# Performance work log

Measured on AMD Instinct MI355X. Metric: run time of the kernel, lower is better.

Reference implementation:

```python
import jax, jax.numpy as jnp
import numpy as np

ALPHA = 0.2  # leaky relu slope
NEG = -1e9


def setup_inputs() -> dict:
    key = jax.random.key(0)
    ks = jax.random.split(key, 8)
    B, N, F_IN, H, HID, OUT = 2, 4096, 512, 4, 128, 64
    x = jax.random.normal(ks[0], (B, N, F_IN), dtype=jnp.float32)
    adj = jax.random.randint(ks[1], (B, N, N), 0, 2, dtype=jnp.int32)
    s_in = float(np.sqrt(2.0 / (F_IN + HID)))
    W_heads = jax.random.normal(ks[2], (H, HID, F_IN), dtype=jnp.float32) * s_in
    a1_heads = jax.random.normal(ks[3], (H, HID), dtype=jnp.float32) * 0.1
    a2_heads = jax.random.normal(ks[4], (H, HID), dtype=jnp.float32) * 0.1
    s_out = float(np.sqrt(2.0 / (H * HID + OUT)))
    W_out = jax.random.normal(ks[5], (OUT, H * HID), dtype=jnp.float32) * s_out
    a1_out = jax.random.normal(ks[6], (OUT,), dtype=jnp.float32) * 0.1
    a2_out = jax.random.normal(ks[7], (OUT,), dtype=jnp.float32) * 0.1
    return {"x": x, "adj": adj, "W_heads": W_heads, "a1_heads": a1_heads,
            "a2_heads": a2_heads, "W_out": W_out, "a1_out": a1_out, "a2_out": a2_out}


def _gat_layer(x, adj, W, a1, a2, concat):
    # x: [B,N,F], W: [O,F], a1/a2: [O]
    h = jnp.einsum('bnf,of->bno', x, W)            # [B,N,O]
    f1 = jnp.einsum('bno,o->bn', h, a1)            # [B,N]
    f2 = jnp.einsum('bno,o->bn', h, a2)            # [B,N]
    e = f1[:, :, None] + f2[:, None, :]            # [B,N,N] additive scores
    e = jnp.where(e > 0, e, ALPHA * e)             # leaky relu
    e = jnp.where(adj == 0, NEG, e)                # adjacency mask
    att = jax.nn.softmax(e, axis=2)
    h_prime = jnp.einsum('bnm,bmo->bno', att, h)
    return jax.nn.elu(h_prime) if concat else h_prime


def reference(x, adj, W_heads, a1_heads, a2_heads, W_out, a1_out, a2_out):
    H = W_heads.shape[0]
    heads = [_gat_layer(x, adj, W_heads[i], a1_heads[i], a2_heads[i], True)
             for i in range(H)]
    x_cat = jnp.concatenate(heads, axis=2)         # [B,N,H*HID]
    return _gat_layer(x_cat, adj, W_out, a1_out, a2_out, False)
```

## Files before the change

kernel.cpp:

```cpp
#include <hip/hip_runtime.h>

#define TB 2
#define TN 4096
#define TH 4
#define THID 128
#define TOUT 64
#define NW 128

using f4    = __attribute__((ext_vector_type(4))) float;
using s16x8 = __attribute__((ext_vector_type(8))) short;
using s16x4 = __attribute__((ext_vector_type(4))) short;
using u32x4 = __attribute__((ext_vector_type(4))) unsigned;

static __device__ __forceinline__ short f2bf(float f){
  unsigned u = __float_as_uint(f);
  unsigned r = u + 0x7FFFu + ((u >> 16) & 1u);
  return (short)(r >> 16);
}
static __device__ __forceinline__ float bf2f(short s){
  return __uint_as_float(((unsigned)(unsigned short)s) << 16);
}
static __device__ __forceinline__ unsigned encf(float f){
  unsigned u = __float_as_uint(f);
  return (u & 0x80000000u) ? ~u : (u | 0x80000000u);
}
static __device__ __forceinline__ float decf(unsigned u){
  unsigned v = (u & 0x80000000u) ? (u & 0x7FFFFFFFu) : ~u;
  return __uint_as_float(v);
}
static __device__ __forceinline__ void gll16(const void* g, void* l){
  __builtin_amdgcn_global_load_lds((const __attribute__((address_space(1))) unsigned int*)g,
                                   (__attribute__((address_space(3))) unsigned int*)l, 16, 0, 0);
}
static __device__ __forceinline__ f4 mfma_bf16(s16x8 a, s16x8 b, f4 c){
  return __builtin_amdgcn_mfma_f32_16x16x32_bf16(a, b, c, 0, 0, 0);
}

__global__ void k_pack(const int* __restrict__ adj, unsigned* __restrict__ adjp){
  int t = blockIdx.x * 256 + threadIdx.x;
  const int4* p = (const int4*)adj + (size_t)t * 8;
  unsigned m = 0;
#pragma unroll
  for (int i = 0; i < 8; ++i){
    int4 v = p[i];
    m |= (v.x != 0 ? 1u : 0u) << (i*4+0);
    m |= (v.y != 0 ? 1u : 0u) << (i*4+1);
    m |= (v.z != 0 ? 1u : 0u) << (i*4+2);
    m |= (v.w != 0 ? 1u : 0u) << (i*4+3);
  }
  adjp[t] = m;
}

__global__ void k_split(const float* __restrict__ x, short* __restrict__ hi, short* __restrict__ lo){
  int t = blockIdx.x * 256 + threadIdx.x;
  f4 v = ((const f4*)x)[t];
  s16x4 h, l;
#pragma unroll
  for (int e = 0; e < 4; ++e){
    short hb = f2bf(v[e]);
    h[e] = hb;
    l[e] = f2bf(v[e] - bf2f(hb));
  }
  ((s16x4*)hi)[t] = h;
  ((s16x4*)lo)[t] = l;
}
__global__ void k_cvt(const float* __restrict__ x, short* __restrict__ o){
  int t = blockIdx.x * 256 + threadIdx.x;
  f4 v = ((const f4*)x)[t];
  s16x4 h;
#pragma unroll
  for (int e = 0; e < 4; ++e) h[e] = f2bf(v[e]);
  ((s16x4*)o)[t] = h;
}

__global__ __launch_bounds__(512, 2) void k_gemm1(
    const short* __restrict__ xh, const short* __restrict__ xl,
    const short* __restrict__ wh, const short* __restrict__ wl,
    const float* __restrict__ a1h, const float* __restrict__ a2h,
    short* __restrict__ hTb, float* __restrict__ f1g,
    float* __restrict__ Qa, float* __restrict__ Sa, unsigned* __restrict__ mx){
  __shared__ short tiles[2][4][8192];
  __shared__ float red[2][128][2];
  __shared__ float bmx[2];
  int tid = threadIdx.x, lane = tid & 63, w = tid >> 6;
  int kgrp = lane >> 4, li = lane & 15;
  int nblk = blockIdx.x >> 6, mblk = blockIdx.x & 63;
  int n0 = nblk * 128, m0 = mblk * 128;
  int wn = w >> 2, wm = w & 3;
  const f4 fz = {0.f, 0.f, 0.f, 0.f};
  f4 acc[4][2];
#pragma unroll
  for (int i = 0; i < 4; ++i)
#pragma unroll
    for (int j = 0; j < 2; ++j) acc[i][j] = fz;

#pragma unroll
  for (int tno = 0; tno < 4; ++tno){
    const short* gb = (tno==0 ? wh : tno==1 ? wl : tno==2 ? xh : xl);
    int r0 = (tno < 2) ? n0 : m0;
#pragma unroll
    for (int i = 0; i < 2; ++i){
      int s = (i*8 + w)*64 + lane;
      int row = s >> 3, c = s & 7, cs = c ^ (row & 7);
      gll16(gb + (size_t)(r0 + row)*512 + cs*8, (char*)tiles[0][tno] + (i*8+w)*1024);
    }
  }
  asm volatile("s_waitcnt vmcnt(0)" ::: "memory");
  __syncthreads();

  for (int kt = 0; kt < 8; ++kt){
    int cur = kt & 1;
    if (kt < 7){
      int k0 = (kt+1) * 64;
#pragma unroll
      for (int tno = 0; tno < 4; ++tno){
        const short* gb = (tno==0 ? wh : tno==1 ? wl : tno==2 ? xh : xl);
        int r0 = (tno < 2) ? n0 : m0;
#pragma unroll
        for (int i = 0; i < 2; ++i){
          int s = (i*8 + w)*64 + lane;
          int row = s >> 3, c = s & 7, cs = c ^ (row & 7);
          gll16(gb + (size_t)(r0 + row)*512 + k0 + cs*8, (char*)tiles[cur^1][tno] + (i*8+w)*1024);
        }
      }
    }
    const char* t0 = (const char*)tiles[cur][0];
    const char* t1 = (const char*)tiles[cur][1];
    const char* t2 = (const char*)tiles[cur][2];
    const char* t3 = (const char*)tiles[cur][3];
#pragma unroll
    for (int ks = 0; ks < 2; ++ks){
      int ck = ks*4 + kgrp;
      s16x8 ah[4], al[4], bh[2], bl[2];
#pragma unroll
      for (int fn = 0; fn < 4; ++fn){
        int row = wn*64 + fn*16 + li;
        int off = row*128 + ((ck ^ (row & 7)) << 4);
        ah[fn] = *(const s16x8*)(t0 + off);
        al[fn] = *(const s16x8*)(t1 + off);
      }
#pragma unroll
      for (int fm = 0; fm < 2; ++fm){
        int row = wm*32 + fm*16 + li;
        int off = row*128 + ((ck ^ (row & 7)) << 4);
        bh[fm] = *(const s16x8*)(t2 + off);
        bl[fm] = *(const s16x8*)(t3 + off);
      }
#pragma unroll
      for (int fn = 0; fn < 4; ++fn)
#pragma unroll
        for (int fm = 0; fm < 2; ++fm)
          acc[fn][fm] = mfma_bf16(ah[fn], bh[fm], acc[fn][fm]);
#pragma unroll
      for (int fn = 0; fn < 4; ++fn)
#pragma unroll
        for (int fm = 0; fm < 2; ++fm)
          acc[fn][fm] = mfma_bf16(ah[fn], bl[fm], acc[fn][fm]);
#pragma unroll
      for (int fn = 0; fn < 4; ++fn)
#pragma unroll
        for (int fm = 0; fm < 2; ++fm)
          acc[fn][fm] = mfma_bf16(al[fn], bh[fm], acc[fn][fm]);
    }
    asm volatile("s_waitcnt vmcnt(0)" ::: "memory");
    __syncthreads();
  }
  int head = nblk;
#pragma unroll
  for (int fn = 0; fn < 4; ++fn){
#pragma unroll
    for (int fm = 0; fm < 2; ++fm){
#pragma unroll
      for (int r = 0; r < 4; ++r){
        int nout = n0 + wn*64 + fn*16 + kgrp*4 + r;
        int m = m0 + wm*32 + fm*16 + li;
        int b = m >> 12, n = m & 4095;
        int hid = nout & 127;
        size_t idx = ((size_t)((b*TH + head)*THID + hid))*TN + n;
        hTb[idx] = f2bf(acc[fn][fm][r]);
      }
    }
  }
  const float* a1p = a1h + head*THID;
  const float* a2p = a2h + head*THID;
  float s1[2] = {0.f, 0.f}, s2[2] = {0.f, 0.f};
#pragma unroll
  for (int fn = 0; fn < 4; ++fn)
#pragma unroll
    for (int r = 0; r < 4; ++r){
      int row = wn*64 + fn*16 + kgrp*4 + r;
      float w1 = a1p[row], w2 = a2p[row];
#pragma unroll
      for (int fm = 0; fm < 2; ++fm){
        s1[fm] = fmaf(acc[fn][fm][r], w1, s1[fm]);
        s2[fm] = fmaf(acc[fn][fm][r], w2, s2[fm]);
      }
    }
#pragma unroll
  for (int fm = 0; fm < 2; ++fm){
    s1[fm] += __shfl_xor(s1[fm], 16); s1[fm] += __shfl_xor(s1[fm], 32);
    s2[fm] += __shfl_xor(s2[fm], 16); s2[fm] += __shfl_xor(s2[fm], 32);
  }
  if (kgrp == 0){
#pragma unroll
    for (int fm = 0; fm < 2; ++fm){
      int col = wm*32 + fm*16 + li;
      red[wn][col][0] = s1[fm];
      red[wn][col][1] = s2[fm];
    }
  }
  __syncthreads();
  if (tid < 128){
    float f1v = red[0][tid][0] + red[1][tid][0];
    float f2v = red[0][tid][1] + red[1][tid][1];
    int m = m0 + tid, b = m >> 12, n = m & 4095;
    int idx = (b*TH + head)*TN + n;
    f1g[idx] = f1v;
    Qa[idx] = expf(f2v);
    Sa[idx] = expf(0.2f*f2v);
    float wmx = f2v;
#pragma unroll
    for (int d = 1; d < 64; d <<= 1) wmx = fmaxf(wmx, __shfl_xor(wmx, d));
    if ((tid & 63) == 0) bmx[tid >> 6] = wmx;
  }
  __syncthreads();
  if (tid == 0){
    int b = m0 >> 12;
    atomicMax(&mx[b*TH + head], encf(fmaxf(bmx[0], bmx[1])));
  }
}

__global__ __launch_bounds__(256, 2) void k_attn1(
    const short* __restrict__ hTb, const float* __restrict__ f1,
    const float* __restrict__ Qa, const float* __restrict__ Sa,
    const unsigned* __restrict__ adjp, const unsigned* __restrict__ mx,
    float* __restrict__ part, float* __restrict__ sums){
  __shared__ short tile[2][8192];
  __shared__ float Qs[2048], Ss[2048];
  int tid = threadIdx.x, lane = tid & 63, w = tid >> 6;
  int kgrp = lane >> 4, li = lane & 15;
  int bid = blockIdx.x;
  int js = bid >> 8, b = (bid >> 7) & 1, h = (bid >> 5) & 3, rblk = bid & 31;
  int bh = b*TH + h;
  int jbase = js * 2048;
  const short* hbase = hTb + ((size_t)bh*THID)*TN;

#pragma unroll
  for (int i = 0; i < 2; ++i){
    gll16(Qa + (size_t)bh*TN + jbase + (i*4+w)*256 + lane*4, (char*)Qs + (i*4+w)*1024);
    gll16(Sa + (size_t)bh*TN + jbase + (i*4+w)*256 + lane*4, (char*)Ss + (i*4+w)*1024);
  }
#pragma unroll
  for (int i = 0; i < 4; ++i){
    int s = (i*4 + w)*64 + lane;
    int row = s >> 3, c = s & 7, cs = c ^ (row & 7);
    gll16(hbase + (size_t)row*TN + jbase + cs*8, (char*)tile[0] + (i*4+w)*1024);
  }
  int r0 = rblk*128 + w*32;
  float Pv[2], Rv[2];
  int rowa[2];
  float mf = decf(mx[bh]);
#pragma unroll
  for (int rf = 0; rf < 2; ++rf){
    int row = r0 + rf*16 + li;
    rowa[rf] = row;
    float f1v = f1[bh*TN + row];
    float e = f1v + mf;
    float m = e > 0.f ? e : 0.2f*e;
    Pv[rf] = expf(f1v - m);
    Rv[rf] = expf(0.2f*f1v - m);
  }
  const f4 fz = {0.f,0.f,0.f,0.f};
  f4 acc[2][8];
#pragma unroll
  for (int i = 0; i < 2; ++i)
#pragma unroll
    for (int j = 0; j < 8; ++j) acc[i][j] = fz;
  f4 accs[2] = {fz, fz};
  s16x8 ones;
#pragma unroll
  for (int e = 0; e < 8; ++e) ones[e] = (short)0x3F80;

  uint2 awc[2], awn[2];
#pragma unroll
  for (int rf = 0; rf < 2; ++rf)
    awc[rf] = *(const uint2*)&adjp[(size_t)(b*TN + rowa[rf])*NW + (jbase >> 5)];

  asm volatile("s_waitcnt vmcnt(0)" ::: "memory");
  __syncthreads();

  for (int jt = 0; jt < 32; ++jt){
    int cur = jt & 1;
    if (jt < 31){
      int jg = jbase + (jt+1)*64;
#pragma unroll
      for (int i = 0; i < 4; ++i){
        int s = (i*4 + w)*64 + lane;
        int row = s >> 3, c = s & 7, cs = c ^ (row & 7);
        gll16(hbase + (size_t)row*TN + jg + cs*8, (char*)tile[cur^1] + (i*4+w)*1024);
      }
    }
    int jn = jt < 31 ? jt+1 : jt;
#pragma unroll
    for (int rf = 0; rf < 2; ++rf)
      awn[rf] = *(const uint2*)&adjp[(size_t)(b*TN + rowa[rf])*NW + ((jbase + jn*64) >> 5)];
    int j0 = jt*64;
    const char* tp = (const char*)tile[cur];
#pragma unroll
    for (int ks = 0; ks < 2; ++ks){
      int jloc = j0 + ks*32 + kgrp*8;
      float qv[8], sv[8];
      *(f4*)&qv[0] = *(const f4*)&Qs[jloc];
      *(f4*)&qv[4] = *(const f4*)&Qs[jloc+4];
      *(f4*)&sv[0] = *(const f4*)&Ss[jloc];
      *(f4*)&sv[4] = *(const f4*)&Ss[jloc+4];
      s16x8 af[2];
#pragma unroll
      for (int rf = 0; rf < 2; ++rf){
        unsigned word = ks ? awc[rf].y : awc[rf].x;
        unsigned byt = (word >> (kgrp*8)) & 0xFFu;
        float P = Pv[rf], R = Rv[rf];
        u32x4 pw;
#pragma unroll
        for (int pe = 0; pe < 4; ++pe){
          float va = fmaxf(P*qv[2*pe],   R*sv[2*pe]);
          float vb = fmaxf(P*qv[2*pe+1], R*sv[2*pe+1]);
          va = (byt & (1u << (2*pe)))   ? va : 0.f;
          vb = (byt & (1u << (2*pe+1))) ? vb : 0.f;
          unsigned ua = __float_as_uint(va) + 0x8000u;
          unsigned ub = __float_as_uint(vb) + 0x8000u;
          pw[pe] = __builtin_amdgcn_perm(ub, ua, 0x07060302);
        }
        af[rf] = __builtin_bit_cast(s16x8, pw);
      }
      accs[0] = mfma_bf16(af[0], ones, accs[0]);
      accs[1] = mfma_bf16(af[1], ones, accs[1]);
#pragma unroll
      for (int cf = 0; cf < 8; ++cf){
        int col = cf*16 + li;
        int off = col*128 + (((ks*4 + kgrp) ^ (col & 7)) << 4);
        s16x8 bfr = *(const s16x8*)(tp + off);
        acc[0][cf] = mfma_bf16(af[0], bfr, acc[0][cf]);
        acc[1][cf] = mfma_bf16(af[1], bfr, acc[1][cf]);
      }
    }
    asm volatile("s_waitcnt vmcnt(0)" ::: "memory");
    __syncthreads();
    awc[0] = awn[0]; awc[1] = awn[1];
  }
  int sl = js*8 + bh;
  if (li == 0){
#pragma unroll
    for (int rf = 0; rf < 2; ++rf)
#pragma unroll
      for (int r = 0; r < 4; ++r)
        sums[(size_t)sl*TN + r0 + rf*16 + kgrp*4 + r] = accs[rf][r];
  }
#pragma unroll
  for (int rf = 0; rf < 2; ++rf)
#pragma unroll
    for (int cf = 0; cf < 8; ++cf)
#pragma unroll
      for (int r = 0; r < 4; ++r){
        int row = r0 + rf*16 + kgrp*4 + r;
        int hid = cf*16 + li;
        part[((size_t)sl*TN + row)*THID + hid] = acc[rf][cf][r];
      }
}

__global__ void k_comb1(const float* __restrict__ part, const float* __restrict__ sums,
                        short* __restrict__ xcat){
  int t = blockIdx.x*256 + threadIdx.x;
  int hid4 = t & 31, n = (t >> 5) & 4095, h = (t >> 17) & 3, b = t >> 19;
  int bh = b*TH + h;
  size_t rowoff = (size_t)bh*TN + n;
  size_t rowoff2 = (size_t)(8 + bh)*TN + n;
  f4 p0 = ((const f4*)part)[rowoff*32 + hid4];
  f4 p1 = ((const f4*)part)[rowoff2*32 + hid4];
  float s = sums[rowoff] + sums[rowoff2];
  f4 v = (p0 + p1) / s;
  s16x4 o;
#pragma unroll
  for (int e = 0; e < 4; ++e){
    float x = v[e];
    o[e] = f2bf(x > 0.f ? x : expm1f(x));
  }
  ((s16x4*)xcat)[(size_t)(b*TN + n)*128 + h*32 + hid4] = o;
}

__global__ __launch_bounds__(128) void k_gemm2(
    const short* __restrict__ xcat, const short* __restrict__ wo,
    const float* __restrict__ a1o, const float* __restrict__ a2o,
    short* __restrict__ h2T, float* __restrict__ f1o,
    float* __restrict__ Q2, float* __restrict__ S2, unsigned* __restrict__ mx2){
  int tid = threadIdx.x, lane = tid & 63, w = tid >> 6;
  int kgrp = lane >> 4, li = lane & 15;
  int m0 = blockIdx.x * 32;
  const f4 fz = {0.f,0.f,0.f,0.f};
  f4 acc[4] = {fz, fz, fz, fz};
  int rowA = m0 + w*16 + li;
  for (int kt = 0; kt < 16; ++kt){
    int k = kt*32 + kgrp*8;
    s16x8 a = *(const s16x8*)(xcat + (size_t)rowA*512 + k);
#pragma unroll
    for (int cf = 0; cf < 4; ++cf){
      int col = cf*16 + li;
      s16x8 bfr = *(const s16x8*)(wo + (size_t)col*512 + k);
      acc[cf] = mfma_bf16(a, bfr, acc[cf]);
    }
  }
  float p1[4] = {0,0,0,0}, p2[4] = {0,0,0,0};
#pragma unroll
  for (int cf = 0; cf < 4; ++cf){
    int o = cf*16 + li;
    float w1 = a1o[o], w2 = a2o[o];
#pragma unroll
    for (int r = 0; r < 4; ++r){
      p1[r] = fmaf(acc[cf][r], w1, p1[r]);
      p2[r] = fmaf(acc[cf][r], w2, p2[r]);
    }
  }
#pragma unroll
  for (int r = 0; r < 4; ++r){
#pragma unroll
    for (int d = 1; d < 16; d <<= 1){
      p1[r] += __shfl_xor(p1[r], d);
      p2[r] += __shfl_xor(p2[r], d);
    }
  }
#pragma unroll
  for (int cf = 0; cf < 4; ++cf)
#pragma unroll
    for (int r = 0; r < 4; ++r){
      int row = m0 + w*16 + kgrp*4 + r;
      int o = cf*16 + li;
      int b = row >> 12, n = row & 4095;
      h2T[((size_t)(b*TOUT + o))*TN + n] = f2bf(acc[cf][r]);
    }
  if (li == 0){
#pragma unroll
    for (int r = 0; r < 4; ++r){
      int row = m0 + w*16 + kgrp*4 + r;
      f1o[row] = p1[r];
      Q2[row] = expf(p2[r]);
      S2[row] = expf(0.2f*p2[r]);
    }
  }
  float m2 = fmaxf(fmaxf(p2[0], p2[1]), fmaxf(p2[2], p2[3]));
  m2 = fmaxf(m2, __shfl_xor(m2, 16));
  m2 = fmaxf(m2, __shfl_xor(m2, 32));
  __shared__ float bm[2];
  if (lane == 0) bm[w] = m2;
  __syncthreads();
  if (tid == 0) atomicMax(&mx2[m0 >> 12], encf(fmaxf(bm[0], bm[1])));
}

__global__ __launch_bounds__(256, 2) void k_attn2(
    const short* __restrict__ h2T, const float* __restrict__ f1o,
    const float* __restrict__ Q2, const float* __restrict__ S2,
    const unsigned* __restrict__ adjp, const unsigned* __restrict__ mx2,
    float* __restrict__ part, float* __restrict__ sums){
  __shared__ short tile[2][4096];
  __shared__ float Qs[512], Ss[512];
  int tid = threadIdx.x, lane = tid & 63, w = tid >> 6;
  int kgrp = lane >> 4, li = lane & 15;
  int bid = blockIdx.x;
  int js = bid >> 6, b = (bid >> 5) & 1, rblk = bid & 31;
  int jbase = js * 512;
  const short* hbase = h2T + (size_t)b*TOUT*TN;

  if (w < 2) gll16(Q2 + (size_t)b*TN + jbase + w*256 + lane*4, (char*)Qs + w*1024);
  else       gll16(S2 + (size_t)b*TN + jbase + (w-2)*256 + lane*4, (char*)Ss + (w-2)*1024);
#pragma unroll
  for (int i = 0; i < 2; ++i){
    int s = (i*4 + w)*64 + lane;
    int row = s >> 3, c = s & 7, cs = c ^ (row & 7);
    gll16(hbase + (size_t)row*TN + jbase + cs*8, (char*)tile[0] + (i*4+w)*1024);
  }
  int r0 = rblk*128 + w*32;
  float Pv[2], Rv[2];
  int rowa[2];
  float mf = decf(mx2[b]);
#pragma unroll
  for (int rf = 0; rf < 2; ++rf){
    int row = r0 + rf*16 + li;
    rowa[rf] = row;
    float f1v = f1o[b*TN + row];
    float e = f1v + mf;
    float m = e > 0.f ? e : 0.2f*e;
    Pv[rf] = expf(f1v - m);
    Rv[rf] = expf(0.2f*f1v - m);
  }
  const f4 fz = {0.f,0.f,0.f,0.f};
  f4 acc[2][4];
#pragma unroll
  for (int i = 0; i < 2; ++i)
#pragma unroll
    for (int j = 0; j < 4; ++j) acc[i][j] = fz;
  f4 accs[2] = {fz, fz};
  s16x8 ones;
#pragma unroll
  for (int e = 0; e < 8; ++e) ones[e] = (short)0x3F80;

  uint2 awc[2], awn[2];
#pragma unroll
  for (int rf = 0; rf < 2; ++rf)
    awc[rf] = *(const uint2*)&adjp[(size_t)(b*TN + rowa[rf])*NW + (jbase >> 5)];

  asm volatile("s_waitcnt vmcnt(0)" ::: "memory");
  __syncthreads();

  for (int jt = 0; jt < 8; ++jt){
    int cur = jt & 1;
    if (jt < 7){
      int jg = jbase + (jt+1)*64;
#pragma unroll
      for (int i = 0; i < 2; ++i){
        int s = (i*4 + w)*64 + lane;
        int row = s >> 3, c = s & 7, cs = c ^ (row & 7);
        gll16(hbase + (size_t)row*TN + jg + cs*8, (char*)tile[cur^1] + (i*4+w)*1024);
      }
    }
    int jn = jt < 7 ? jt+1 : jt;
#pragma unroll
    for (int rf = 0; rf < 2; ++rf)
      awn[rf] = *(const uint2*)&adjp[(size_t)(b*TN + rowa[rf])*NW + ((jbase + jn*64) >> 5)];
    int j0 = jt*64;
    const char* tp = (const char*)tile[cur];
#pragma unroll
    for (int ks = 0; ks < 2; ++ks){
      int jloc = j0 + ks*32 + kgrp*8;
      float qv[8], sv[8];
      *(f4*)&qv[0] = *(const f4*)&Qs[jloc];
      *(f4*)&qv[4] = *(const f4*)&Qs[jloc+4];
      *(f4*)&sv[0] = *(const f4*)&Ss[jloc];
      *(f4*)&sv[4] = *(const f4*)&Ss[jloc+4];
      s16x8 af[2];
#pragma unroll
      for (int rf = 0; rf < 2; ++rf){
        unsigned word = ks ? awc[rf].y : awc[rf].x;
        unsigned byt = (word >> (kgrp*8)) & 0xFFu;
        float P = Pv[rf], R = Rv[rf];
        u32x4 pw;
#pragma unroll
        for (int pe = 0; pe < 4; ++pe){
          float va = fmaxf(P*qv[2*pe],   R*sv[2*pe]);
          float vb = fmaxf(P*qv[2*pe+1], R*sv[2*pe+1]);
          va = (byt & (1u << (2*pe)))   ? va : 0.f;
          vb = (byt & (1u << (2*pe+1))) ? vb : 0.f;
          unsigned ua = __float_as_uint(va) + 0x8000u;
          unsigned ub = __float_as_uint(vb) + 0x8000u;
          pw[pe] = __builtin_amdgcn_perm(ub, ua, 0x07060302);
        }
        af[rf] = __builtin_bit_cast(s16x8, pw);
      }
      accs[0] = mfma_bf16(af[0], ones, accs[0]);
      accs[1] = mfma_bf16(af[1], ones, accs[1]);
#pragma unroll
      for (int cf = 0; cf < 4; ++cf){
        int col = cf*16 + li;
        int off = col*128 + (((ks*4 + kgrp) ^ (col & 7)) << 4);
        s16x8 bfr = *(const s16x8*)(tp + off);
        acc[0][cf] = mfma_bf16(af[0], bfr, acc[0][cf]);
        acc[1][cf] = mfma_bf16(af[1], bfr, acc[1][cf]);
      }
    }
    asm volatile("s_waitcnt vmcnt(0)" ::: "memory");
    __syncthreads();
    awc[0] = awn[0]; awc[1] = awn[1];
  }
  int sl = js*2 + b;
  if (li == 0){
#pragma unroll
    for (int rf = 0; rf < 2; ++rf)
#pragma unroll
      for (int r = 0; r < 4; ++r)
        sums[(size_t)sl*TN + r0 + rf*16 + kgrp*4 + r] = accs[rf][r];
  }
#pragma unroll
  for (int rf = 0; rf < 2; ++rf)
#pragma unroll
    for (int cf = 0; cf < 4; ++cf)
#pragma unroll
      for (int r = 0; r < 4; ++r){
        int row = r0 + rf*16 + kgrp*4 + r;
        int o = cf*16 + li;
        part[((size_t)sl*TN + row)*TOUT + o] = acc[rf][cf][r];
      }
}

__global__ void k_comb2(const float* __restrict__ part, const float* __restrict__ sums,
                        float* __restrict__ out){
  int t = blockIdx.x*256 + threadIdx.x;
  int o4 = t & 15, n = (t >> 4) & 4095, b = t >> 16;
  f4 a = {0.f,0.f,0.f,0.f};
  float s = 0.f;
#pragma unroll
  for (int js = 0; js < 8; ++js){
    int sl = js*2 + b;
    a += ((const f4*)part)[((size_t)sl*TN + n)*16 + o4];
    s += sums[(size_t)sl*TN + n];
  }
  f4 r = a / s;
  ((f4*)out)[((size_t)(b*TN + n))*16 + o4] = r;
}

extern "C" void kernel_launch(void* const* d_in, const int* in_sizes, int n_in,
                              void* d_out, int out_size, void* d_ws, size_t ws_size,
                              hipStream_t stream) {
  (void)in_sizes; (void)n_in; (void)out_size; (void)ws_size;
  const float* x       = (const float*)d_in[0];
  const int*   adj     = (const int*)d_in[1];
  const float* W_heads = (const float*)d_in[2];
  const float* a1h     = (const float*)d_in[3];
  const float* a2h     = (const float*)d_in[4];
  const float* W_out   = (const float*)d_in[5];
  const float* a1o     = (const float*)d_in[6];
  const float* a2o     = (const float*)d_in[7];

  char* p = (char*)d_ws;
  auto alloc = [&](size_t sz){ char* r = p; p += (sz + 255) & ~(size_t)255; return r; };
  unsigned* adjp  = (unsigned*) alloc(4ull*1048576);
  short*    wo    = (short*)    alloc(2ull*32768);
  short*    hTb   = (short*)    alloc(2ull*4194304);
  float*    f1    = (float*)    alloc(4ull*32768);
  float*    Qa    = (float*)    alloc(4ull*32768);
  float*    Sa    = (float*)    alloc(4ull*32768);
  unsigned* mx    = (unsigned*) alloc(4ull*16);
  short*    xcat  = (short*)    alloc(2ull*4194304);
  float*    f1o   = (float*)    alloc(4ull*8192);
  float*    Q2    = (float*)    alloc(4ull*8192);
  float*    S2    = (float*)    alloc(4ull*8192);
  short*    h2T   = (short*)    alloc(2ull*524288);
  float*    sums1 = (float*)    alloc(4ull*65536);
  float*    sums2 = (float*)    alloc(4ull*65536);
  char* A = alloc(33554432ull);
  short* xh   = (short*)A;
  short* xl   = (short*)(A + 8388608);
  float* part1 = (float*)A;
  char* Bu = alloc(16777216ull);
  short* wh = (short*)Bu;
  short* wl = (short*)(Bu + 524288);
  float* part2 = (float*)Bu;

  k_pack <<<4096, 256, 0, stream>>>(adj, adjp);
  k_split<<<4096, 256, 0, stream>>>(x, xh, xl);
  k_split<<<256, 256, 0, stream>>>(W_heads, wh, wl);
  k_cvt  <<<32, 256, 0, stream>>>(W_out, wo);
  hipMemsetAsync(mx, 0, 64, stream);
  k_gemm1<<<256, 512, 0, stream>>>(xh, xl, wh, wl, a1h, a2h, hTb, f1, Qa, Sa, mx);
  k_attn1<<<512, 256, 0, stream>>>(hTb, f1, Qa, Sa, adjp, mx, part1, sums1);
  k_comb1<<<4096, 256, 0, stream>>>(part1, sums1, xcat);
  k_gemm2<<<256, 128, 0, stream>>>(xcat, wo, a1o, a2o, h2T, f1o, Q2, S2, mx + 8);
  k_attn2<<<512, 256, 0, stream>>>(h2T, f1o, Q2, S2, adjp, mx + 8, part2, sums2);
  k_comb2<<<512, 256, 0, stream>>>(part2, sums2, (float*)d_out);
}
```

Measured before the change: 153.9 us.

## Split attention kernels into more blocks, store layer-1 partials as bf16

Layer-1 attention now splits the neighbor dimension into four 1024-wide chunks instead of two, which doubles the grid to 1024 blocks and raises the occupancy hint to 4. Its partial sums are stored as bf16, and the combine kernel reduces four bf16 partials with 8-wide vector loads. Layer-2 attention uses one 16-row fragment per wave instead of two, which also doubles its grid. The mx memset is folded into k_pack to remove one API call. The aim is better GPU fill and less partial-buffer traffic, at the cost of more partial reductions and bf16 rounding of the unnormalized partial accumulators.

Result: no change. 154.5 us (+0.4%).

```diff
diff --git a/kernel.cpp b/kernel.cpp
--- a/kernel.cpp
+++ b/kernel.cpp
@@ -36,7 +36,9 @@
   return __builtin_amdgcn_mfma_f32_16x16x32_bf16(a, b, c, 0, 0, 0);
 }
 
-__global__ void k_pack(const int* __restrict__ adj, unsigned* __restrict__ adjp){
+__global__ void k_pack(const int* __restrict__ adj, unsigned* __restrict__ adjp,
+                       unsigned* __restrict__ mx){
+  if (blockIdx.x == 0 && threadIdx.x < 16) mx[threadIdx.x] = 0;
   int t = blockIdx.x * 256 + threadIdx.x;
   const int4* p = (const int4*)adj + (size_t)t * 8;
   unsigned m = 0;
@@ -230,26 +232,23 @@
   }
 }
 
-__global__ __launch_bounds__(256, 2) void k_attn1(
+__global__ __launch_bounds__(256, 4) void k_attn1(
     const short* __restrict__ hTb, const float* __restrict__ f1,
     const float* __restrict__ Qa, const float* __restrict__ Sa,
     const unsigned* __restrict__ adjp, const unsigned* __restrict__ mx,
-    float* __restrict__ part, float* __restrict__ sums){
+    short* __restrict__ part, float* __restrict__ sums){
   __shared__ short tile[2][8192];
-  __shared__ float Qs[2048], Ss[2048];
+  __shared__ float Qs[1024], Ss[1024];
   int tid = threadIdx.x, lane = tid & 63, w = tid >> 6;
   int kgrp = lane >> 4, li = lane & 15;
   int bid = blockIdx.x;
   int js = bid >> 8, b = (bid >> 7) & 1, h = (bid >> 5) & 3, rblk = bid & 31;
   int bh = b*TH + h;
-  int jbase = js * 2048;
+  int jbase = js * 1024;
   const short* hbase = hTb + ((size_t)bh*THID)*TN;
 
-#pragma unroll
-  for (int i = 0; i < 2; ++i){
-    gll16(Qa + (size_t)bh*TN + jbase + (i*4+w)*256 + lane*4, (char*)Qs + (i*4+w)*1024);
-    gll16(Sa + (size_t)bh*TN + jbase + (i*4+w)*256 + lane*4, (char*)Ss + (i*4+w)*1024);
-  }
+  gll16(Qa + (size_t)bh*TN + jbase + w*256 + lane*4, (char*)Qs + w*1024);
+  gll16(Sa + (size_t)bh*TN + jbase + w*256 + lane*4, (char*)Ss + w*1024);
 #pragma unroll
   for (int i = 0; i < 4; ++i){
     int s = (i*4 + w)*64 + lane;
@@ -289,9 +288,9 @@
   asm volatile("s_waitcnt vmcnt(0)" ::: "memory");
   __syncthreads();
 
-  for (int jt = 0; jt < 32; ++jt){
+  for (int jt = 0; jt < 16; ++jt){
     int cur = jt & 1;
-    if (jt < 31){
+    if (jt < 15){
       int jg = jbase + (jt+1)*64;
 #pragma unroll
       for (int i = 0; i < 4; ++i){
@@ -300,7 +299,7 @@
         gll16(hbase + (size_t)row*TN + jg + cs*8, (char*)tile[cur^1] + (i*4+w)*1024);
       }
     }
-    int jn = jt < 31 ? jt+1 : jt;
+    int jn = jt < 15 ? jt+1 : jt;
 #pragma unroll
     for (int rf = 0; rf < 2; ++rf)
       awn[rf] = *(const uint2*)&adjp[(size_t)(b*TN + rowa[rf])*NW + ((jbase + jn*64) >> 5)];
@@ -364,28 +363,33 @@
       for (int r = 0; r < 4; ++r){
         int row = r0 + rf*16 + kgrp*4 + r;
         int hid = cf*16 + li;
-        part[((size_t)sl*TN + row)*THID + hid] = acc[rf][cf][r];
-      }
-}
-
-__global__ void k_comb1(const float* __restrict__ part, const float* __restrict__ sums,
+        part[((size_t)sl*TN + row)*THID + hid] = f2bf(acc[rf][cf][r]);
+      }
+}
+
+__global__ void k_comb1(const short* __restrict__ part, const float* __restrict__ sums,
                         short* __restrict__ xcat){
   int t = blockIdx.x*256 + threadIdx.x;
-  int hid4 = t & 31, n = (t >> 5) & 4095, h = (t >> 17) & 3, b = t >> 19;
+  int hid8 = t & 15, n = (t >> 4) & 4095, h = (t >> 16) & 3, b = t >> 18;
   int bh = b*TH + h;
-  size_t rowoff = (size_t)bh*TN + n;
-  size_t rowoff2 = (size_t)(8 + bh)*TN + n;
-  f4 p0 = ((const f4*)part)[rowoff*32 + hid4];
-  f4 p1 = ((const f4*)part)[rowoff2*32 + hid4];
-  float s = sums[rowoff] + sums[rowoff2];
-  f4 v = (p0 + p1) / s;
-  s16x4 o;
-#pragma unroll
-  for (int e = 0; e < 4; ++e){
-    float x = v[e];
+  float a[8] = {0,0,0,0,0,0,0,0};
+  float s = 0.f;
+#pragma unroll
+  for (int js = 0; js < 4; ++js){
+    size_t rowoff = (size_t)(js*8 + bh)*TN + n;
+    s16x8 pv = *(const s16x8*)(part + rowoff*THID + hid8*8);
+#pragma unroll
+    for (int e = 0; e < 8; ++e) a[e] += bf2f(pv[e]);
+    s += sums[rowoff];
+  }
+  float inv = 1.f / s;
+  s16x8 o;
+#pragma unroll
+  for (int e = 0; e < 8; ++e){
+    float x = a[e] * inv;
     o[e] = f2bf(x > 0.f ? x : expm1f(x));
   }
-  ((s16x4*)xcat)[(size_t)(b*TN + n)*128 + h*32 + hid4] = o;
+  *(s16x8*)(xcat + ((size_t)(b*TN + n))*512 + h*128 + hid8*8) = o;
 }
 
 __global__ __launch_bounds__(128) void k_gemm2(
@@ -455,7 +459,7 @@
   if (tid == 0) atomicMax(&mx2[m0 >> 12], encf(fmaxf(bm[0], bm[1])));
 }
 
-__global__ __launch_bounds__(256, 2) void k_attn2(
+__global__ __launch_bounds__(256, 4) void k_attn2(
     const short* __restrict__ h2T, const float* __restrict__ f1o,
     const float* __restrict__ Q2, const float* __restrict__ S2,
     const unsigned* __restrict__ adjp, const unsigned* __restrict__ mx2,
@@ -465,7 +469,7 @@
   int tid = threadIdx.x, lane = tid & 63, w = tid >> 6;
   int kgrp = lane >> 4, li = lane & 15;
   int bid = blockIdx.x;
-  int js = bid >> 6, b = (bid >> 5) & 1, rblk = bid & 31;
+  int js = bid >> 7, b = (bid >> 6) & 1, rblk = bid & 63;
   int jbase = js * 512;
   const short* hbase = h2T + (size_t)b*TOUT*TN;
 
@@ -477,35 +481,23 @@
     int row = s >> 3, c = s & 7, cs = c ^ (row & 7);
     gll16(hbase + (size_t)row*TN + jbase + cs*8, (char*)tile[0] + (i*4+w)*1024);
   }
-  int r0 = rblk*128 + w*32;
-  float Pv[2], Rv[2];
-  int rowa[2];
+  int r0 = rblk*64 + w*16;
+  int rowa = r0 + li;
   float mf = decf(mx2[b]);
-#pragma unroll
-  for (int rf = 0; rf < 2; ++rf){
-    int row = r0 + rf*16 + li;
-    rowa[rf] = row;
-    float f1v = f1o[b*TN + row];
-    float e = f1v + mf;
-    float m = e > 0.f ? e : 0.2f*e;
-    Pv[rf] = expf(f1v - m);
-    Rv[rf] = expf(0.2f*f1v - m);
-  }
+  float f1v = f1o[b*TN + rowa];
+  float e0 = f1v + mf;
+  float m0v = e0 > 0.f ? e0 : 0.2f*e0;
+  float Pv = expf(f1v - m0v);
+  float Rv = expf(0.2f*f1v - m0v);
   const f4 fz = {0.f,0.f,0.f,0.f};
-  f4 acc[2][4];
-#pragma unroll
-  for (int i = 0; i < 2; ++i)
-#pragma unroll
-    for (int j = 0; j < 4; ++j) acc[i][j] = fz;
-  f4 accs[2] = {fz, fz};
+  f4 acc[4] = {fz, fz, fz, fz};
+  f4 accs = fz;
   s16x8 ones;
 #pragma unroll
   for (int e = 0; e < 8; ++e) ones[e] = (short)0x3F80;
 
-  uint2 awc[2], awn[2];
-#pragma unroll
-  for (int rf = 0; rf < 2; ++rf)
-    awc[rf] = *(const uint2*)&adjp[(size_t)(b*TN + rowa[rf])*NW + (jbase >> 5)];
+  uint2 awc, awn;
+  awc = *(const uint2*)&adjp[(size_t)(b*TN + rowa)*NW + (jbase >> 5)];
 
   asm volatile("s_waitcnt vmcnt(0)" ::: "memory");
   __syncthreads();
@@ -522,9 +514,7 @@
       }
     }
     int jn = jt < 7 ? jt+1 : jt;
-#pragma unroll
-    for (int rf = 0; rf < 2; ++rf)
-      awn[rf] = *(const uint2*)&adjp[(size_t)(b*TN + rowa[rf])*NW + ((jbase + jn*64) >> 5)];
+    awn = *(const uint2*)&adjp[(size_t)(b*TN + rowa)*NW + ((jbase + jn*64) >> 5)];
     int j0 = jt*64;
     const char* tp = (const char*)tile[cur];
 #pragma unroll
@@ -535,58 +525,47 @@
       *(f4*)&qv[4] = *(const f4*)&Qs[jloc+4];
       *(f4*)&sv[0] = *(const f4*)&Ss[jloc];
       *(f4*)&sv[4] = *(const f4*)&Ss[jloc+4];
-      s16x8 af[2];
-#pragma unroll
-      for (int rf = 0; rf < 2; ++rf){
-        unsigned word = ks ? awc[rf].y : awc[rf].x;
-        unsigned byt = (word >> (kgrp*8)) & 0xFFu;
-        float P = Pv[rf], R = Rv[rf];
-        u32x4 pw;
-#pragma unroll
-        for (int pe = 0; pe < 4; ++pe){
-          float va = fmaxf(P*qv[2*pe],   R*sv[2*pe]);
-          float vb = fmaxf(P*qv[2*pe+1], R*sv[2*pe+1]);
-          va = (byt & (1u << (2*pe)))   ? va : 0.f;
-          vb = (byt & (1u << (2*pe+1))) ? vb : 0.f;
-          unsigned ua = __float_as_uint(va) + 0x8000u;
-          unsigned ub = __float_as_uint(vb) + 0x8000u;
-          pw[pe] = __builtin_amdgcn_perm(ub, ua, 0x07060302);
-        }
-        af[rf] = __builtin_bit_cast(s16x8, pw);
-      }
-      accs[0] = mfma_bf16(af[0], ones, accs[0]);
-      accs[1] = mfma_bf16(af[1], ones, accs[1]);
+      unsigned word = ks ? awc.y : awc.x;
+      unsigned byt = (word >> (kgrp*8)) & 0xFFu;
+      u32x4 pw;
+#pragma unroll
+      for (int pe = 0; pe < 4; ++pe){
+        float va = fmaxf(Pv*qv[2*pe],   Rv*sv[2*pe]);
+        float vb = fmaxf(Pv*qv[2*pe+1], Rv*sv[2*pe+1]);
+        va = (byt & (1u << (2*pe)))   ? va : 0.f;
+        vb = (byt & (1u << (2*pe+1))) ? vb : 0.f;
+        unsigned ua = __float_as_uint(va) + 0x8000u;
+        unsigned ub = __float_as_uint(vb) + 0x8000u;
+        pw[pe] = __builtin_amdgcn_perm(ub, ua, 0x07060302);
+      }
+      s16x8 af = __builtin_bit_cast(s16x8, pw);
+      accs = mfma_bf16(af, ones, accs);
 #pragma unroll
       for (int cf = 0; cf < 4; ++cf){
         int col = cf*16 + li;
         int off = col*128 + (((ks*4 + kgrp) ^ (col & 7)) << 4);
         s16x8 bfr = *(const s16x8*)(tp + off);
-        acc[0][cf] = mfma_bf16(af[0], bfr, acc[0][cf]);
-        acc[1][cf] = mfma_bf16(af[1], bfr, acc[1][cf]);
+        acc[cf] = mfma_bf16(af, bfr, acc[cf]);
       }
     }
     asm volatile("s_waitcnt vmcnt(0)" ::: "memory");
     __syncthreads();
-    awc[0] = awn[0]; awc[1] = awn[1];
+    awc = awn;
   }
   int sl = js*2 + b;
   if (li == 0){
 #pragma unroll
-    for (int rf = 0; rf < 2; ++rf)
-#pragma unroll
-      for (int r = 0; r < 4; ++r)
-        sums[(size_t)sl*TN + r0 + rf*16 + kgrp*4 + r] = accs[rf][r];
-  }
-#pragma unroll
-  for (int rf = 0; rf < 2; ++rf)
-#pragma unroll
-    for (int cf = 0; cf < 4; ++cf)
-#pragma unroll
-      for (int r = 0; r < 4; ++r){
-        int row = r0 + rf*16 + kgrp*4 + r;
-        int o = cf*16 + li;
-        part[((size_t)sl*TN + row)*TOUT + o] = acc[rf][cf][r];
-      }
+    for (int r = 0; r < 4; ++r)
+      sums[(size_t)sl*TN + r0 + kgrp*4 + r] = accs[r];
+  }
+#pragma unroll
+  for (int cf = 0; cf < 4; ++cf)
+#pragma unroll
+    for (int r = 0; r < 4; ++r){
+      int row = r0 + kgrp*4 + r;
+      int o = cf*16 + li;
+      part[((size_t)sl*TN + row)*TOUT + o] = acc[cf][r];
+    }
 }
 
 __global__ void k_comb2(const float* __restrict__ part, const float* __restrict__ sums,
@@ -632,26 +611,25 @@
   float*    Q2    = (float*)    alloc(4ull*8192);
   float*    S2    = (float*)    alloc(4ull*8192);
   short*    h2T   = (short*)    alloc(2ull*524288);
-  float*    sums1 = (float*)    alloc(4ull*65536);
+  float*    sums1 = (float*)    alloc(4ull*131072);
   float*    sums2 = (float*)    alloc(4ull*65536);
   char* A = alloc(33554432ull);
   short* xh   = (short*)A;
   short* xl   = (short*)(A + 8388608);
-  float* part1 = (float*)A;
+  short* part1 = (short*)A;
   char* Bu = alloc(16777216ull);
   short* wh = (short*)Bu;
   short* wl = (short*)(Bu + 524288);
   float* part2 = (float*)Bu;
 
-  k_pack <<<4096, 256, 0, stream>>>(adj, adjp);
+  k_pack <<<4096, 256, 0, stream>>>(adj, adjp, mx);
   k_split<<<4096, 256, 0, stream>>>(x, xh, xl);
   k_split<<<256, 256, 0, stream>>>(W_heads, wh, wl);
   k_cvt  <<<32, 256, 0, stream>>>(W_out, wo);
-  hipMemsetAsync(mx, 0, 64, stream);
   k_gemm1<<<256, 512, 0, stream>>>(xh, xl, wh, wl, a1h, a2h, hTb, f1, Qa, Sa, mx);
-  k_attn1<<<512, 256, 0, stream>>>(hTb, f1, Qa, Sa, adjp, mx, part1, sums1);
-  k_comb1<<<4096, 256, 0, stream>>>(part1, sums1, xcat);
+  k_attn1<<<1024, 256, 0, stream>>>(hTb, f1, Qa, Sa, adjp, mx, part1, sums1);
+  k_comb1<<<2048, 256, 0, stream>>>(part1, sums1, xcat);
   k_gemm2<<<256, 128, 0, stream>>>(xcat, wo, a1o, a2o, h2T, f1o, Q2, S2, mx + 8);
-  k_attn2<<<512, 256, 0, stream>>>(h2T, f1o, Q2, S2, adjp, mx + 8, part2, sums2);
+  k_attn2<<<1024, 256, 0, stream>>>(h2T, f1o, Q2, S2, adjp, mx + 8, part2, sums2);
   k_comb2<<<512, 256, 0, stream>>>(part2, sums2, (float*)d_out);
 }
```
